# Performance work log

Measured on AMD Instinct MI355X. Metric: run time of the kernel, lower is better.

Reference implementation:

```python
import jax, jax.numpy as jnp
import numpy as np

N, D, DH, H = 2048, 256, 256, 4
DHEAD = DH // H
NEG = -1e30


def setup_inputs() -> dict:
    key = jax.random.key(0)
    ks = jax.random.split(key, 24)
    s = 0.05
    inp = {
        'axiom_states': jax.random.normal(ks[0], (N, D), jnp.float32),
        'adj0': (jax.random.uniform(ks[1], (N, N)) < 0.015).astype(jnp.float32),
        'adj1': (jax.random.uniform(ks[2], (N, N)) < 0.015).astype(jnp.float32),
        'w0': jax.random.uniform(ks[3], (N, N), jnp.float32),
        'w1': jax.random.uniform(ks[4], (N, N), jnp.float32),
        'Wm0': jax.random.normal(ks[5], (DH, D), jnp.float32) * s,
        'bm0': jax.random.normal(ks[6], (DH,), jnp.float32) * s,
        'Wa0': jax.random.normal(ks[7], (H, 2 * D), jnp.float32) * s,
        'ba0': jax.random.normal(ks[8], (H,), jnp.float32) * s,
        'Wm1': jax.random.normal(ks[9], (DH, D), jnp.float32) * s,
        'bm1': jax.random.normal(ks[10], (DH,), jnp.float32) * s,
        'Wa1': jax.random.normal(ks[11], (H, 2 * D), jnp.float32) * s,
        'ba1': jax.random.normal(ks[12], (H,), jnp.float32) * s,
        'gru_wih': jax.random.normal(ks[13], (3 * D, 2 * DH), jnp.float32) * s,
        'gru_whh': jax.random.normal(ks[14], (3 * D, D), jnp.float32) * s,
        'gru_bih': jax.random.normal(ks[15], (3 * D,), jnp.float32) * s,
        'gru_bhh': jax.random.normal(ks[16], (3 * D,), jnp.float32) * s,
        'ln_g': jnp.ones((D,), jnp.float32),
        'ln_b': jnp.zeros((D,), jnp.float32),
    }
    return inp


def _edge_messages(x, adj, w, Wm, bm, Wa, ba):
    # GAT-style decomposition of Linear([x_i, x_j]) -> a_cur[i] + a_nb[j] + b
    a_cur = x @ Wa[:, :D].T                      # [N,H] (target i, first half of concat)
    a_nb = x @ Wa[:, D:].T                       # [N,H] (neighbor j, second half)
    s = a_nb[:, None, :] + a_cur[None, :, :] + ba  # [j,i,H]
    s = jax.nn.leaky_relu(s, 0.2)
    s = s * w[:, :, None]                        # edge-weight scaled scores (pre-softmax)
    mask = adj != 0                              # edge j -> i iff adj[j,i] != 0
    logits = jnp.where(mask[:, :, None], s, NEG)
    attn = jax.nn.softmax(logits, axis=0) * mask[:, :, None]  # zero for isolated nodes
    msg = (x @ Wm.T + bm).reshape(N, H, DHEAD)   # per-neighbor messages
    agg = jnp.einsum('jih,jhd->ihd', attn, msg)  # softmax-weighted sum over neighbors
    return agg.reshape(N, DH)


def _forward(axiom_states, adj0, adj1, w0, w1, Wm0, bm0, Wa0, ba0,
             Wm1, bm1, Wa1, ba1, gru_wih, gru_whh, gru_bih, gru_bhh, ln_g, ln_b):
    m0 = _edge_messages(axiom_states, adj0, w0, Wm0, bm0, Wa0, ba0)
    m1 = _edge_messages(axiom_states, adj1, w1, Wm1, bm1, Wa1, ba1)
    msg = jnp.concatenate([m0, m1], axis=-1)     # dropout is identity in eval
    # GRUCell (torch semantics)
    gi = msg @ gru_wih.T + gru_bih
    gh = axiom_states @ gru_whh.T + gru_bhh
    r = jax.nn.sigmoid(gi[:, :D] + gh[:, :D])
    z = jax.nn.sigmoid(gi[:, D:2 * D] + gh[:, D:2 * D])
    n = jnp.tanh(gi[:, 2 * D:] + r * gh[:, 2 * D:])
    h = (1.0 - z) * n + z * axiom_states
    # LayerNorm
    mu = jnp.mean(h, axis=-1, keepdims=True)
    var = jnp.var(h, axis=-1, keepdims=True)
    return (h - mu) * jax.lax.rsqrt(var + 1e-5) * ln_g + ln_b


def reference(axiom_states, adj0, adj1, w0, w1, Wm0, bm0, Wa0, ba0,
              Wm1, bm1, Wa1, ba1, gru_wih, gru_whh, gru_bih, gru_bhh, ln_g, ln_b):
    return _forward(axiom_states, adj0, adj1, w0, w1, Wm0, bm0, Wa0, ba0,
                    Wm1, bm1, Wa1, ba1, gru_wih, gru_whh, gru_bih, gru_bhh, ln_g, ln_b)
```

## Files before the change

kernel.cpp:

```cpp
#include <hip/hip_runtime.h>

#define NN 2048
#define DD 256
#define HH 4
#define PW 1280
#define ECAP 128

typedef unsigned short ushort_t;
typedef __attribute__((ext_vector_type(4))) unsigned short us4;
typedef __attribute__((ext_vector_type(8))) short s8;
typedef __attribute__((ext_vector_type(4))) float f4;

__device__ __forceinline__ ushort_t f2b(float f) {
    unsigned int u = __float_as_uint(f);
    return (ushort_t)((u + 0x7fffu + ((u >> 16) & 1u)) >> 16);
}
__device__ __forceinline__ float b2f(ushort_t b) {
    return __uint_as_float(((unsigned int)b) << 16);
}
__device__ __forceinline__ void gl_lds16(const void* g, void* l) {
    __builtin_amdgcn_global_load_lds(
        (const __attribute__((address_space(1))) void*)g,
        (__attribute__((address_space(3))) void*)l, 16, 0, 0);
}

__global__ __launch_bounds__(256) void zero_cnt(int* __restrict__ cnt)
{
    const int id = blockIdx.x * 256 + threadIdx.x;
    if (id < 2 * NN) cnt[id] = 0;
}

#define E_EB  2048
#define E_XC  2560
#define E_WC  2880
#define E_WI  3264
#define E_NB  3392

__global__ __launch_bounds__(256) void prep_kernel(
    const float* __restrict__ x,
    const float* __restrict__ adj0, const float* __restrict__ adj1,
    const float* __restrict__ w0, const float* __restrict__ w1,
    const float* __restrict__ Wm0, const float* __restrict__ Wm1,
    const float* __restrict__ whh, const float* __restrict__ wih,
    const float* __restrict__ Wa0, const float* __restrict__ Wa1,
    int* __restrict__ cnt, uint2* __restrict__ ejw,
    ushort_t* __restrict__ xb, ushort_t* __restrict__ Wcatb, ushort_t* __restrict__ wihb,
    float* __restrict__ acur, float* __restrict__ anb)
{
    __shared__ float sh[16][257];
    const int b = blockIdx.x, t = threadIdx.x;

    if (b < E_EB) {
        const int j = b;
        const float4* a0p = (const float4*)(adj0 + (size_t)j * NN);
        const float4* a1p = (const float4*)(adj1 + (size_t)j * NN);
        const float4* w0p = (const float4*)(w0 + (size_t)j * NN);
        const float4* w1p = (const float4*)(w1 + (size_t)j * NN);
        const float4 a00 = a0p[t], a01 = a0p[t + 256];
        const float4 a10 = a1p[t], a11 = a1p[t + 256];
        const float4 q00 = w0p[t], q01 = w0p[t + 256];
        const float4 q10 = w1p[t], q11 = w1p[t + 256];

        #pragma unroll
        for (int l = 0; l < 2; ++l) {
            #pragma unroll
            for (int half = 0; half < 2; ++half) {
                const float4 a = l ? (half ? a11 : a10) : (half ? a01 : a00);
                const float4 q = l ? (half ? q11 : q10) : (half ? q01 : q00);
                const float av[4] = {a.x, a.y, a.z, a.w};
                const float qv[4] = {q.x, q.y, q.z, q.w};
                const int i0 = (t + half * 256) * 4;
                #pragma unroll
                for (int u = 0; u < 4; ++u) {
                    if (av[u] != 0.f) {
                        const int i = i0 + u;
                        const int slot = atomicAdd(&cnt[l * NN + i], 1);
                        if (slot >= 0 && slot < ECAP) {
                            uint2 pk;
                            pk.x = (unsigned int)j;
                            pk.y = __float_as_uint(qv[u]);
                            ejw[((size_t)l * NN + i) * ECAP + slot] = pk;
                        }
                    }
                }
            }
        }
        return;
    }
    if (b < E_XC) {
        const int id = (b - E_EB) * 1024 + t * 4;
        const float4 v = *(const float4*)(x + id);
        us4 o; o.x = f2b(v.x); o.y = f2b(v.y); o.z = f2b(v.z); o.w = f2b(v.w);
        *(us4*)(xb + id) = o;
        return;
    }
    if (b < E_WC) {
        const int id = (b - E_XC) * 1024 + t * 4;
        const int c = id >> 8, k = id & 255;
        const float* src = (c < 256) ? Wm0 + (size_t)c * DD + k
                         : (c < 512) ? Wm1 + (size_t)(c - 256) * DD + k
                                     : whh + (size_t)(c - 512) * DD + k;
        const float4 v = *(const float4*)src;
        us4 o; o.x = f2b(v.x); o.y = f2b(v.y); o.z = f2b(v.z); o.w = f2b(v.w);
        *(us4*)(Wcatb + id) = o;
        return;
    }
    if (b < E_WI) {
        const int id = (b - E_WC) * 1024 + t * 4;
        const float4 v = *(const float4*)(wih + id);
        us4 o; o.x = f2b(v.x); o.y = f2b(v.y); o.z = f2b(v.z); o.w = f2b(v.w);
        *(us4*)(wihb + id) = o;
        return;
    }
    {
        const int i0 = (b - E_WI) * 16;
        for (int rr = 0; rr < 16; ++rr)
            sh[rr][t] = x[(size_t)(i0 + rr) * DD + t];
        __syncthreads();
        const int r = t >> 4, idx = t & 15;
        const int l = idx >> 3, isnb = (idx >> 2) & 1, h = idx & 3;
        const float* wrow = (l ? Wa1 : Wa0) + h * (2 * DD) + isnb * DD;
        float acc = 0.f;
        for (int k = 0; k < DD; ++k) acc = fmaf(sh[r][k], wrow[k], acc);
        float* dst = isnb ? anb : acur;
        dst[((size_t)l * NN + i0 + r) * HH + h] = acc;
    }
}

__device__ __forceinline__ void gemm_core(
    const ushort_t* __restrict__ A, int lda, const ushort_t* __restrict__ B, int ldb,
    int r0, int c0, int K, ushort_t (*as)[64], ushort_t (*bs)[64], f4 acc[2][2])
{
    const int t = threadIdx.x;
    const int wave = t >> 6, lane = t & 63;
    const int wm = (wave & 1) * 32, wn = (wave >> 1) * 32;
    const int fm = lane & 15, fq = lane >> 4;

    const int m0q0 = wave * 16 + (lane >> 3);
    const int m0q1 = m0q0 + 8;
    const int cs0 = ((lane & 7) ^ (m0q0 & 7)) * 8;
    const int cs1 = ((lane & 7) ^ (m0q1 & 7)) * 8;
    const ushort_t* ga0 = A + (size_t)(r0 + m0q0) * lda + cs0;
    const ushort_t* ga1 = A + (size_t)(r0 + m0q1) * lda + cs1;
    const ushort_t* gb0 = B + (size_t)(c0 + m0q0) * ldb + cs0;
    const ushort_t* gb1 = B + (size_t)(c0 + m0q1) * ldb + cs1;
    ushort_t* la0 = &as[wave * 16][0];
    ushort_t* la1 = &as[wave * 16 + 8][0];
    ushort_t* lb0 = &bs[wave * 16][0];
    ushort_t* lb1 = &bs[wave * 16 + 8][0];
    const int ra0 = wm + fm, ra1 = wm + 16 + fm;
    const int rb0 = wn + fm, rb1 = wn + 16 + fm;

    for (int k0 = 0; k0 < K; k0 += 64) {
        __syncthreads();
        gl_lds16(ga0 + k0, la0);
        gl_lds16(ga1 + k0, la1);
        gl_lds16(gb0 + k0, lb0);
        gl_lds16(gb1 + k0, lb1);
        __syncthreads();
        #pragma unroll
        for (int kk = 0; kk < 2; ++kk) {
            const int cc = kk * 4 + fq;
            const s8 a0 = *(const s8*)&as[ra0][(cc ^ (ra0 & 7)) * 8];
            const s8 a1 = *(const s8*)&as[ra1][(cc ^ (ra1 & 7)) * 8];
            const s8 b0 = *(const s8*)&bs[rb0][(cc ^ (rb0 & 7)) * 8];
            const s8 b1 = *(const s8*)&bs[rb1][(cc ^ (rb1 & 7)) * 8];
            acc[0][0] = __builtin_amdgcn_mfma_f32_16x16x32_bf16(a0, b0, acc[0][0], 0, 0, 0);
            acc[0][1] = __builtin_amdgcn_mfma_f32_16x16x32_bf16(a0, b1, acc[0][1], 0, 0, 0);
            acc[1][0] = __builtin_amdgcn_mfma_f32_16x16x32_bf16(a1, b0, acc[1][0], 0, 0, 0);
            acc[1][1] = __builtin_amdgcn_mfma_f32_16x16x32_bf16(a1, b1, acc[1][1], 0, 0, 0);
        }
    }
}

__global__ __launch_bounds__(256) void gemm1_kernel(
    const ushort_t* __restrict__ xb, const ushort_t* __restrict__ Wcatb,
    const float* __restrict__ bm0, const float* __restrict__ bm1,
    const float* __restrict__ bhh,
    ushort_t* __restrict__ msgb, float* __restrict__ gh)
{
    __shared__ ushort_t as[64][64];
    __shared__ ushort_t bs[64][64];
    const int t = threadIdx.x;
    const int wave = t >> 6, lane = t & 63;
    const int wm = (wave & 1) * 32, wn = (wave >> 1) * 32;
    const int fm = lane & 15, fq = lane >> 4;
    const int c0 = blockIdx.x * 64, r0 = blockIdx.y * 64;
    f4 acc[2][2] = {};
    gemm_core(xb, DD, Wcatb, DD, r0, c0, DD, as, bs, acc);
    #pragma unroll
    for (int ni = 0; ni < 2; ++ni) {
        const int col = c0 + wn + ni * 16 + fm;
        const float bv = (col < 256) ? bm0[col]
                       : (col < 512) ? bm1[col - 256]
                                     : bhh[col - 512];
        #pragma unroll
        for (int mi = 0; mi < 2; ++mi) {
            #pragma unroll
            for (int r = 0; r < 4; ++r) {
                const int row = r0 + wm + mi * 16 + fq * 4 + r;
                const float v = acc[mi][ni][r] + bv;
                if (col < 512) msgb[(size_t)row * 512 + col] = f2b(v);
                else           gh[(size_t)row * 768 + col - 512] = v;
            }
        }
    }
}

__global__ __launch_bounds__(256) void attn_kernel(
    const int* __restrict__ cnt, const uint2* __restrict__ ejw,
    const float* __restrict__ acur, const float* __restrict__ anb,
    const float* __restrict__ ba0, const float* __restrict__ ba1,
    const ushort_t* __restrict__ msgb, ushort_t* __restrict__ mcatb)
{
    const int i = blockIdx.x, l = blockIdx.y, t = threadIdx.x;
    __shared__ float es[HH][ECAP];
    __shared__ int ejs[ECAP];
    const int ne = min(max(cnt[l * NN + i], 0), ECAP);
    const float* ba = l ? ba1 : ba0;
    const size_t ebase = ((size_t)l * NN + i) * ECAP;

    if (t < ne) {
        const uint2 pk = ejw[ebase + t];
        const int j = (int)pk.x;
        const float wv = __uint_as_float(pk.y);
        ejs[t] = j;
        const float4 av = *(const float4*)(anb + ((size_t)l * NN + j) * HH);
        const float sv[4] = {av.x, av.y, av.z, av.w};
        #pragma unroll
        for (int h = 0; h < HH; ++h) {
            float s = sv[h] + acur[((size_t)l * NN + i) * HH + h] + ba[h];
            s = (s > 0.f) ? s : 0.2f * s;
            es[h][t] = s * wv;
        }
    }
    __syncthreads();
    {
        const int h = t >> 6, lane = t & 63;
        float s0 = (lane < ne) ? es[h][lane] : -1e30f;
        float s1 = (lane + 64 < ne) ? es[h][lane + 64] : -1e30f;
        float m = fmaxf(s0, s1);
        #pragma unroll
        for (int off = 32; off; off >>= 1) m = fmaxf(m, __shfl_xor(m, off));
        const float p0 = expf(s0 - m), p1 = expf(s1 - m);
        float sum = p0 + p1;
        #pragma unroll
        for (int off = 32; off; off >>= 1) sum += __shfl_xor(sum, off);
        const float inv = (ne > 0) ? 1.f / sum : 0.f;
        es[h][lane] = p0 * inv;
        if (lane + 64 < ECAP) es[h][lane + 64] = p1 * inv;
    }
    __syncthreads();
    const int h = t >> 6;
    const int off = l * DD + t;
    float acc = 0.f;
    int e = 0;
    for (; e + 4 <= ne; e += 4) {
        const float v0 = b2f(msgb[(size_t)ejs[e + 0] * 512 + off]);
        const float v1 = b2f(msgb[(size_t)ejs[e + 1] * 512 + off]);
        const float v2 = b2f(msgb[(size_t)ejs[e + 2] * 512 + off]);
        const float v3 = b2f(msgb[(size_t)ejs[e + 3] * 512 + off]);
        acc = fmaf(es[h][e + 0], v0, acc);
        acc = fmaf(es[h][e + 1], v1, acc);
        acc = fmaf(es[h][e + 2], v2, acc);
        acc = fmaf(es[h][e + 3], v3, acc);
    }
    for (; e < ne; ++e)
        acc = fmaf(es[h][e], b2f(msgb[(size_t)ejs[e] * 512 + off]), acc);
    mcatb[(size_t)i * (2 * DD) + off] = f2b(acc);
}

__global__ __launch_bounds__(256) void gemm2_kernel(
    const ushort_t* __restrict__ mcatb, const ushort_t* __restrict__ wihb,
    const float* __restrict__ bih, float* __restrict__ gi)
{
    __shared__ ushort_t as[64][64];
    __shared__ ushort_t bs[64][64];
    const int t = threadIdx.x;
    const int wave = t >> 6, lane = t & 63;
    const int wm = (wave & 1) * 32, wn = (wave >> 1) * 32;
    const int fm = lane & 15, fq = lane >> 4;
    const int c0 = blockIdx.x * 64, r0 = blockIdx.y * 64;
    f4 acc[2][2] = {};
    gemm_core(mcatb, 512, wihb, 512, r0, c0, 512, as, bs, acc);
    #pragma unroll
    for (int ni = 0; ni < 2; ++ni) {
        const int col = c0 + wn + ni * 16 + fm;
        const float bv = bih[col];
        #pragma unroll
        for (int mi = 0; mi < 2; ++mi)
            #pragma unroll
            for (int r = 0; r < 4; ++r)
                gi[(size_t)(r0 + wm + mi * 16 + fq * 4 + r) * 768 + col] =
                    acc[mi][ni][r] + bv;
    }
}

__global__ __launch_bounds__(256) void gates_ln(
    const float* __restrict__ gi, const float* __restrict__ gh, const float* __restrict__ x,
    const float* __restrict__ lng, const float* __restrict__ lnb, float* __restrict__ out)
{
    __shared__ float rs1[4], rs2[4];
    const int t = threadIdx.x;
    const int r0 = blockIdx.x * 4;
    const float gv = lng[t], bv = lnb[t];
    float hv[4];
    #pragma unroll
    for (int r = 0; r < 4; ++r) {
        const int row = r0 + r;
        const float gir = gi[(size_t)row * 768 + t];
        const float giz = gi[(size_t)row * 768 + 256 + t];
        const float gin = gi[(size_t)row * 768 + 512 + t];
        const float ghr = gh[(size_t)row * 768 + t];
        const float ghz = gh[(size_t)row * 768 + 256 + t];
        const float ghn = gh[(size_t)row * 768 + 512 + t];
        const float rr = 1.f / (1.f + expf(-(gir + ghr)));
        const float zz = 1.f / (1.f + expf(-(giz + ghz)));
        const float nn = tanhf(gin + rr * ghn);
        hv[r] = (1.f - zz) * nn + zz * x[(size_t)row * DD + t];
    }
    const int lane = t & 63, wid = t >> 6;
    for (int r = 0; r < 4; ++r) {
        float s1 = hv[r], s2 = hv[r] * hv[r];
        #pragma unroll
        for (int off = 32; off; off >>= 1) {
            s1 += __shfl_down(s1, off);
            s2 += __shfl_down(s2, off);
        }
        if (lane == 0) { rs1[wid] = s1; rs2[wid] = s2; }
        __syncthreads();
        const float sum = rs1[0] + rs1[1] + rs1[2] + rs1[3];
        const float sq  = rs2[0] + rs2[1] + rs2[2] + rs2[3];
        const float mu  = sum * (1.f / DD);
        const float var = sq * (1.f / DD) - mu * mu;
        const float inv = rsqrtf(var + 1e-5f);
        out[(size_t)(r0 + r) * DD + t] = (hv[r] - mu) * inv * gv + bv;
        __syncthreads();
    }
}

extern "C" void kernel_launch(void* const* d_in, const int* in_sizes, int n_in,
                              void* d_out, int out_size, void* d_ws, size_t ws_size,
                              hipStream_t stream)
{
    const float* x    = (const float*)d_in[0];
    const float* adj0 = (const float*)d_in[1];
    const float* adj1 = (const float*)d_in[2];
    const float* w0   = (const float*)d_in[3];
    const float* w1   = (const float*)d_in[4];
    const float* Wm0  = (const float*)d_in[5];
    const float* bm0  = (const float*)d_in[6];
    const float* Wa0  = (const float*)d_in[7];
    const float* ba0  = (const float*)d_in[8];
    const float* Wm1  = (const float*)d_in[9];
    const float* bm1  = (const float*)d_in[10];
    const float* Wa1  = (const float*)d_in[11];
    const float* ba1  = (const float*)d_in[12];
    const float* wih  = (const float*)d_in[13];
    const float* whh  = (const float*)d_in[14];
    const float* bih  = (const float*)d_in[15];
    const float* bhh  = (const float*)d_in[16];
    const float* lng  = (const float*)d_in[17];
    const float* lnb  = (const float*)d_in[18];
    float* out = (float*)d_out;

    float* ws = (float*)d_ws;
    float* gh   = ws;            ws += (size_t)NN * 768;
    float* gi   = ws;            ws += (size_t)NN * 768;
    float* acur = ws;            ws += 2 * NN * HH;
    float* anb  = ws;            ws += 2 * NN * HH;
    int*   cnt  = (int*)ws;      ws += 2 * NN;
    uint2* ejw  = (uint2*)ws;    ws += 2 * 2 * NN * ECAP;
    ushort_t* xb    = (ushort_t*)ws;  ws += (size_t)NN * DD / 2;
    ushort_t* Wcatb = (ushort_t*)ws;  ws += (size_t)PW * DD / 2;
    ushort_t* wihb  = (ushort_t*)ws;  ws += (size_t)768 * 512 / 2;
    ushort_t* msgb  = (ushort_t*)ws;  ws += (size_t)NN * 512 / 2;
    ushort_t* mcatb = (ushort_t*)ws;  ws += (size_t)NN * 512 / 2;

    zero_cnt<<<16, 256, 0, stream>>>(cnt);
    prep_kernel<<<E_NB, 256, 0, stream>>>(
        x, adj0, adj1, w0, w1, Wm0, Wm1, whh, wih, Wa0, Wa1,
        cnt, ejw, xb, Wcatb, wihb, acur, anb);
    gemm1_kernel<<<dim3(PW / 64, NN / 64), 256, 0, stream>>>(
        xb, Wcatb, bm0, bm1, bhh, msgb, gh);
    attn_kernel<<<dim3(NN, 2), 256, 0, stream>>>(
        cnt, ejw, acur, anb, ba0, ba1, msgb, mcatb);
    gemm2_kernel<<<dim3(12, 32), 256, 0, stream>>>(mcatb, wihb, bih, gi);
    gates_ln<<<NN / 4, 256, 0, stream>>>(gi, gh, x, lng, lnb, out);
}
```

Before: 193.0 us.

## Build edge lists per column chunk with LDS counters, drop zero kernel

Edge-list construction now gives each block a 16-column slice of one layer's adjacency and walks all source rows. Counting uses shared-memory atomics instead of global atomics, and the final counts are written directly, which removes the separate zero_cnt launch. Each block now does 32 strided 64-byte row reads instead of contiguous full rows, and the grid for this phase drops from 2048 blocks to 256 blocks. This may reduce memory coalescing and parallelism in exchange for cheaper atomics and one fewer launch.

Measured after the change: 189.6 us. Within noise of the previous version (-1.8%).

```diff
diff --git a/kernel.cpp b/kernel.cpp
--- a/kernel.cpp
+++ b/kernel.cpp
@@ -24,17 +24,11 @@
         (__attribute__((address_space(3))) void*)l, 16, 0, 0);
 }
 
-__global__ __launch_bounds__(256) void zero_cnt(int* __restrict__ cnt)
-{
-    const int id = blockIdx.x * 256 + threadIdx.x;
-    if (id < 2 * NN) cnt[id] = 0;
-}
-
-#define E_EB  2048
-#define E_XC  2560
-#define E_WC  2880
-#define E_WI  3264
-#define E_NB  3392
+#define E_EB  256
+#define E_XC  768
+#define E_WC  1088
+#define E_WI  1472
+#define E_NB  1600
 
 __global__ __launch_bounds__(256) void prep_kernel(
     const float* __restrict__ x,
@@ -51,40 +45,37 @@
     const int b = blockIdx.x, t = threadIdx.x;
 
     if (b < E_EB) {
-        const int j = b;
-        const float4* a0p = (const float4*)(adj0 + (size_t)j * NN);
-        const float4* a1p = (const float4*)(adj1 + (size_t)j * NN);
-        const float4* w0p = (const float4*)(w0 + (size_t)j * NN);
-        const float4* w1p = (const float4*)(w1 + (size_t)j * NN);
-        const float4 a00 = a0p[t], a01 = a0p[t + 256];
-        const float4 a10 = a1p[t], a11 = a1p[t + 256];
-        const float4 q00 = w0p[t], q01 = w0p[t + 256];
-        const float4 q10 = w1p[t], q11 = w1p[t + 256];
-
-        #pragma unroll
-        for (int l = 0; l < 2; ++l) {
+        const int l = b & 1, chunk = b >> 1;
+        const int i0 = chunk * 16;
+        const float* adj = l ? adj1 : adj0;
+        const float* w   = l ? w1 : w0;
+        int* lcnt = (int*)sh;
+        if (t < 16) lcnt[t] = 0;
+        __syncthreads();
+        const int rowLane = t >> 2, q = t & 3;
+        #pragma unroll 2
+        for (int r0r = 0; r0r < NN; r0r += 64) {
+            const int j = r0r + rowLane;
+            const float4 a  = *(const float4*)(adj + (size_t)j * NN + i0 + q * 4);
+            const float4 qw = *(const float4*)(w   + (size_t)j * NN + i0 + q * 4);
+            const float av[4] = {a.x, a.y, a.z, a.w};
+            const float qv[4] = {qw.x, qw.y, qw.z, qw.w};
             #pragma unroll
-            for (int half = 0; half < 2; ++half) {
-                const float4 a = l ? (half ? a11 : a10) : (half ? a01 : a00);
-                const float4 q = l ? (half ? q11 : q10) : (half ? q01 : q00);
-                const float av[4] = {a.x, a.y, a.z, a.w};
-                const float qv[4] = {q.x, q.y, q.z, q.w};
-                const int i0 = (t + half * 256) * 4;
-                #pragma unroll
-                for (int u = 0; u < 4; ++u) {
-                    if (av[u] != 0.f) {
-                        const int i = i0 + u;
-                        const int slot = atomicAdd(&cnt[l * NN + i], 1);
-                        if (slot >= 0 && slot < ECAP) {
-                            uint2 pk;
-                            pk.x = (unsigned int)j;
-                            pk.y = __float_as_uint(qv[u]);
-                            ejw[((size_t)l * NN + i) * ECAP + slot] = pk;
-                        }
+            for (int u = 0; u < 4; ++u) {
+                if (av[u] != 0.f) {
+                    const int li = q * 4 + u;
+                    const int slot = atomicAdd(&lcnt[li], 1);
+                    if (slot < ECAP) {
+                        uint2 pk;
+                        pk.x = (unsigned int)j;
+                        pk.y = __float_as_uint(qv[u]);
+                        ejw[((size_t)l * NN + i0 + li) * ECAP + slot] = pk;
                     }
                 }
             }
         }
+        __syncthreads();
+        if (t < 16) cnt[l * NN + i0 + t] = lcnt[t];
         return;
     }
     if (b < E_XC) {
@@ -377,7 +368,6 @@
     ushort_t* msgb  = (ushort_t*)ws;  ws += (size_t)NN * 512 / 2;
     ushort_t* mcatb = (ushort_t*)ws;  ws += (size_t)NN * 512 / 2;
 
-    zero_cnt<<<16, 256, 0, stream>>>(cnt);
     prep_kernel<<<E_NB, 256, 0, stream>>>(
         x, adj0, adj1, w0, w1, Wm0, Wm1, whh, wih, Wa0, Wa1,
         cnt, ejw, xb, Wcatb, wihb, acur, anb);
```
